# Kernel optimization log

Measured on AMD Instinct MI355X. Metric: run time of the kernel, lower is better.

## Reference

```python
import jax, jax.numpy as jnp
import numpy as np

NUM_HEADS = 16
D_MODEL = 1024
D_K = 64
D_V = 64
NEG_INF = -1e9


def setup_inputs() -> dict:
    key = jax.random.key(0)
    ks = jax.random.split(key, 7)
    B, S = 2, 2048
    Q = jax.random.normal(ks[0], (B, S, D_MODEL), dtype=jnp.float32)
    K = jax.random.normal(ks[1], (B, S, D_MODEL), dtype=jnp.float32)
    V = jax.random.normal(ks[2], (B, S, D_MODEL), dtype=jnp.float32)
    s = 1.0 / np.sqrt(D_MODEL)
    W_q = jax.random.normal(ks[3], (D_MODEL, D_K * NUM_HEADS), dtype=jnp.float32) * s
    W_k = jax.random.normal(ks[4], (D_MODEL, D_K), dtype=jnp.float32) * s
    W_v = jax.random.normal(ks[5], (D_MODEL, D_V), dtype=jnp.float32) * s
    W_o = jax.random.normal(ks[6], (D_V * NUM_HEADS, D_MODEL), dtype=jnp.float32) * (1.0 / np.sqrt(D_V * NUM_HEADS))
    return {"Q": Q, "K": K, "V": V, "W_q": W_q, "W_k": W_k, "W_v": W_v, "W_o": W_o}


def reference(Q, K, V, W_q, W_k, W_v, W_o):
    B, Sq, _ = Q.shape
    Sk = K.shape[1]
    # projections: Q -> per-head, K/V -> single shared head (MQA)
    q = (Q @ W_q).reshape(B, Sq, NUM_HEADS, D_K).transpose(0, 2, 1, 3)  # [B,H,Sq,Dk]
    k = K @ W_k  # [B,Sk,Dk]
    v = V @ W_v  # [B,Sk,Dv]
    scores = jnp.einsum('bhqd,bkd->bhqk', q, k) / jnp.sqrt(jnp.float32(D_K))
    causal = jnp.tril(jnp.ones((Sq, Sk), dtype=bool))  # [Sq,Sk]
    scores = jnp.where(causal[None, None], scores, NEG_INF)
    attn = jax.nn.softmax(scores, axis=-1)  # [B,H,Sq,Sk]
    out = jnp.einsum('bhqk,bkd->bhqd', attn, v)  # [B,H,Sq,Dv]
    out = out.transpose(0, 2, 1, 3).reshape(B, Sq, NUM_HEADS * D_V)
    return out @ W_o
```

## Files before the change

### kernel.cpp

```cpp
#include <hip/hip_runtime.h>
#include <hip/hip_bf16.h>
#include <cstdint>

typedef __bf16 bf16_t;
typedef __bf16 bf16x8 __attribute__((ext_vector_type(8)));
typedef __bf16 bf16x4 __attribute__((ext_vector_type(4)));
typedef float  floatx4 __attribute__((ext_vector_type(4)));

__device__ __forceinline__ bf16_t f2bf(float x) { return (bf16_t)x; }

__device__ __forceinline__ void gll16(const void* g, void* l) {
  __builtin_amdgcn_global_load_lds((const __attribute__((address_space(1))) void*)g,
                                   (__attribute__((address_space(3))) void*)l, 16, 0, 0);
}

#define S_LEN 2048
#define NHEAD 16
#define NTILE 32

__global__ __launch_bounds__(256) void transpose_w2(const float* __restrict__ W0,
                                                    const float* __restrict__ W1,
                                                    bf16_t* __restrict__ O0,
                                                    bf16_t* __restrict__ O1,
                                                    int K, int N) {
  const float* W = blockIdx.z ? W1 : W0;
  bf16_t* Wt = blockIdx.z ? O1 : O0;
  __shared__ float tile[32][33];
  int n0 = blockIdx.x * 32, k0 = blockIdx.y * 32;
  int tx = threadIdx.x & 31, ty = threadIdx.x >> 5;
#pragma unroll
  for (int r = 0; r < 4; ++r)
    tile[ty + 8 * r][tx] = W[(size_t)(k0 + ty + 8 * r) * N + n0 + tx];
  __syncthreads();
#pragma unroll
  for (int r = 0; r < 4; ++r)
    Wt[(size_t)(n0 + ty + 8 * r) * K + k0 + tx] = f2bf(tile[tx][ty + 8 * r]);
}

template <int OUTMODE, bool A_FP32>
__global__ __launch_bounds__(256, 2) void gemm_async(const void* __restrict__ Ain,
                                                     const bf16_t* __restrict__ Bt,
                                                     void* __restrict__ Cout,
                                                     int M, int N, int K) {
  constexpr int BK = 64;
  __shared__ __align__(16) bf16_t As[64 * BK];
  __shared__ __align__(16) bf16_t Bs[128 * BK];
  const int tid = threadIdx.x;
  const int wave = tid >> 6, lane = tid & 63;
  const int quad = lane >> 4, lm = lane & 15;
  const int wr = wave >> 1, wc = wave & 1;
  const int m0 = blockIdx.x * 64, n0 = blockIdx.y * 128;

  floatx4 acc[2][4];
#pragma unroll
  for (int i = 0; i < 2; ++i)
#pragma unroll
    for (int j = 0; j < 4; ++j) acc[i][j] = (floatx4){0.f, 0.f, 0.f, 0.f};

  for (int k0 = 0; k0 < K; k0 += BK) {
    if constexpr (A_FP32) {
#pragma unroll
      for (int rd = 0; rd < 2; ++rd) {
        int idx = rd * 256 + tid, row = idx >> 3, ch = (idx & 7) ^ (row & 7);
        const float* src = (const float*)Ain + (size_t)(m0 + row) * K + k0 + ch * 8;
        float4 f0 = *(const float4*)src;
        float4 f1 = *(const float4*)(src + 4);
        bf16x8 o;
        o[0] = f2bf(f0.x); o[1] = f2bf(f0.y); o[2] = f2bf(f0.z); o[3] = f2bf(f0.w);
        o[4] = f2bf(f1.x); o[5] = f2bf(f1.y); o[6] = f2bf(f1.z); o[7] = f2bf(f1.w);
        *(bf16x8*)&As[idx * 8] = o;
      }
    } else {
#pragma unroll
      for (int rd = 0; rd < 2; ++rd) {
        int idx = rd * 256 + tid, row = idx >> 3, ch = (idx & 7) ^ (row & 7);
        gll16((const bf16_t*)Ain + (size_t)(m0 + row) * K + k0 + ch * 8,
              As + (rd * 256 + wave * 64) * 8);
      }
    }
#pragma unroll
    for (int rd = 0; rd < 4; ++rd) {
      int idx = rd * 256 + tid, row = idx >> 3, ch = (idx & 7) ^ (row & 7);
      gll16(Bt + (size_t)(n0 + row) * K + k0 + ch * 8,
            Bs + (rd * 256 + wave * 64) * 8);
    }
    __syncthreads();
    const int sw = lm & 7;
    bf16x8 af[2][2], bfr[4][2];
#pragma unroll
    for (int i = 0; i < 2; ++i) {
      const bf16_t* base = &As[(wr * 32 + i * 16 + lm) * BK];
      af[i][0] = *(const bf16x8*)(base + ((quad ^ sw) * 8));
      af[i][1] = *(const bf16x8*)(base + (((4 + quad) ^ sw) * 8));
    }
#pragma unroll
    for (int j = 0; j < 4; ++j) {
      const bf16_t* base = &Bs[(wc * 64 + j * 16 + lm) * BK];
      bfr[j][0] = *(const bf16x8*)(base + ((quad ^ sw) * 8));
      bfr[j][1] = *(const bf16x8*)(base + (((4 + quad) ^ sw) * 8));
    }
#pragma unroll
    for (int ks = 0; ks < 2; ++ks)
#pragma unroll
      for (int i = 0; i < 2; ++i)
#pragma unroll
        for (int j = 0; j < 4; ++j)
          acc[i][j] = __builtin_amdgcn_mfma_f32_16x16x32_bf16(af[i][ks], bfr[j][ks],
                                                              acc[i][j], 0, 0, 0);
    __syncthreads();
  }
#pragma unroll
  for (int i = 0; i < 2; ++i) {
#pragma unroll
    for (int j = 0; j < 4; ++j) {
      int row0 = m0 + wr * 32 + i * 16 + quad * 4;
      int col = n0 + wc * 64 + j * 16 + lm;
#pragma unroll
      for (int r = 0; r < 4; ++r) {
        if constexpr (OUTMODE == 3)
          ((bf16_t*)Cout)[(size_t)(row0 + r) * N + col] = f2bf(acc[i][j][r] * 0.125f);
        else
          ((float*)Cout)[(size_t)(row0 + r) * N + col] = acc[i][j][r];
      }
    }
  }
}

__global__ __launch_bounds__(256) void gemm_kv(const float* __restrict__ Kin,
                                               const float* __restrict__ Vin,
                                               const bf16_t* __restrict__ Wkt,
                                               const bf16_t* __restrict__ Wvt,
                                               bf16_t* __restrict__ kp,
                                               bf16_t* __restrict__ vpt,
                                               int M, int K) {
  constexpr int BK = 32, LDK = 40, N = 64;
  const int isV = blockIdx.z;
  const float* A32 = isV ? Vin : Kin;
  const bf16_t* Bt = isV ? Wvt : Wkt;
  __shared__ __align__(16) bf16_t As[64 * LDK];
  __shared__ __align__(16) bf16_t Bs[64 * LDK];
  const int tid = threadIdx.x;
  const int wave = tid >> 6, lane = tid & 63;
  const int quad = lane >> 4, lm = lane & 15;
  const int wr = wave >> 1, wc = wave & 1;
  const int m0 = blockIdx.x * 64;

  floatx4 acc[2][2];
#pragma unroll
  for (int i = 0; i < 2; ++i)
#pragma unroll
    for (int j = 0; j < 2; ++j) acc[i][j] = (floatx4){0.f, 0.f, 0.f, 0.f};

  for (int k0 = 0; k0 < K; k0 += BK) {
    {
      int row = tid >> 2, c8 = tid & 3;
      const float* src = A32 + (size_t)(m0 + row) * K + k0 + c8 * 8;
      float4 f0 = *(const float4*)src;
      float4 f1 = *(const float4*)(src + 4);
      bf16x8 o;
      o[0] = f2bf(f0.x); o[1] = f2bf(f0.y); o[2] = f2bf(f0.z); o[3] = f2bf(f0.w);
      o[4] = f2bf(f1.x); o[5] = f2bf(f1.y); o[6] = f2bf(f1.z); o[7] = f2bf(f1.w);
      *(bf16x8*)&As[row * LDK + c8 * 8] = o;
    }
    {
      int row = tid >> 2, c8 = tid & 3;
      *(bf16x8*)&Bs[row * LDK + c8 * 8] =
          *(const bf16x8*)(Bt + (size_t)row * K + k0 + c8 * 8);
    }
    __syncthreads();
    bf16x8 af[2], bfr[2];
#pragma unroll
    for (int i = 0; i < 2; ++i)
      af[i] = *(const bf16x8*)&As[(wr * 32 + i * 16 + lm) * LDK + quad * 8];
#pragma unroll
    for (int j = 0; j < 2; ++j)
      bfr[j] = *(const bf16x8*)&Bs[(wc * 32 + j * 16 + lm) * LDK + quad * 8];
#pragma unroll
    for (int i = 0; i < 2; ++i)
#pragma unroll
      for (int j = 0; j < 2; ++j)
        acc[i][j] = __builtin_amdgcn_mfma_f32_16x16x32_bf16(af[i], bfr[j],
                                                            acc[i][j], 0, 0, 0);
    __syncthreads();
  }
#pragma unroll
  for (int i = 0; i < 2; ++i) {
#pragma unroll
    for (int j = 0; j < 2; ++j) {
      int row0 = m0 + wr * 32 + i * 16 + quad * 4;
      int col = wc * 32 + j * 16 + lm;
      if (isV) {
        bf16x4 o;
#pragma unroll
        for (int r = 0; r < 4; ++r) o[r] = f2bf(acc[i][j][r]);
        *(bf16x4*)&vpt[(size_t)col * M + row0] = o;
      } else {
#pragma unroll
        for (int r = 0; r < 4; ++r)
          kp[(size_t)(row0 + r) * N + col] = f2bf(acc[i][j][r]);
      }
    }
  }
}

__global__ __launch_bounds__(128, 2) void flash_mqa(const bf16_t* __restrict__ q,
                                                    const bf16_t* __restrict__ kk,
                                                    const bf16_t* __restrict__ vt,
                                                    bf16_t* __restrict__ O,
                                                    int BStot) {
  const int qt = NTILE - 1 - blockIdx.x;
  const int hb = blockIdx.y, b = blockIdx.z;
  const int tid = threadIdx.x;
  const int wave = tid >> 6, lane = tid & 63;
  const int quad = lane >> 4, lm = lane & 15;
  const int h = hb * 2 + wave;

  __shared__ __align__(16) bf16_t k_lds[2][64 * 64];
  __shared__ __align__(16) bf16_t v_lds[2][64 * 64];
  __shared__ __align__(16) bf16_t p_lds[2][64 * 64];

  const size_t bS = (size_t)b * S_LEN;
  const int qb = qt * 64;
  const int sw = lm & 7;

  bf16x8 qf[4][2];
#pragma unroll
  for (int m = 0; m < 4; ++m) {
    const bf16_t* qp = q + (bS + qb + m * 16 + lm) * 1024 + h * 64;
    qf[m][0] = *(const bf16x8*)(qp + quad * 8);
    qf[m][1] = *(const bf16x8*)(qp + 32 + quad * 8);
  }
  bf16x8 onesf;
#pragma unroll
  for (int j = 0; j < 8; ++j) onesf[j] = f2bf(1.0f);

  floatx4 acc[4][4];
  floatx4 ps[4];
#pragma unroll
  for (int m = 0; m < 4; ++m) {
    ps[m] = (floatx4){0.f, 0.f, 0.f, 0.f};
#pragma unroll
    for (int t = 0; t < 4; ++t) acc[m][t] = (floatx4){0.f, 0.f, 0.f, 0.f};
  }

  const int stid = tid;
  bf16x8 kst[4], vst[4];
  auto load_kv = [&](int kt) {
    const int k0 = kt * 64;
#pragma unroll
    for (int it = 0; it < 4; ++it) {
      int idx = it * 128 + stid, r = idx >> 3, c8 = idx & 7;
      kst[it] = *(const bf16x8*)(kk + (bS + k0 + r) * 64 + c8 * 8);
      vst[it] = *(const bf16x8*)(vt + (size_t)r * BStot + bS + k0 + c8 * 8);
    }
  };
  auto write_kv = [&](int buf) {
#pragma unroll
    for (int it = 0; it < 4; ++it) {
      int idx = it * 128 + stid, r = idx >> 3, c8 = idx & 7;
      int addr = r * 64 + ((c8 ^ (r & 7)) * 8);
      *(bf16x8*)&k_lds[buf][addr] = kst[it];
      *(bf16x8*)&v_lds[buf][addr] = vst[it];
    }
  };

  load_kv(0);
  write_kv(0);
  __syncthreads();

  for (int kt = 0; kt <= qt; ++kt) {
    const int cur = kt & 1;
    if (kt < qt) load_kv(kt + 1);

    const bool diag = (kt == qt);
#pragma unroll
    for (int t = 0; t < 4; ++t) {
      const bf16_t* kb = &k_lds[cur][(t * 16 + lm) * 64];
      bf16x8 a0 = *(const bf16x8*)(kb + ((quad ^ sw) * 8));
      bf16x8 a1 = *(const bf16x8*)(kb + (((4 + quad) ^ sw) * 8));
      floatx4 s[4];
#pragma unroll
      for (int m = 0; m < 4; ++m) {
        floatx4 cc = (floatx4){0.f, 0.f, 0.f, 0.f};
        cc = __builtin_amdgcn_mfma_f32_16x16x32_bf16(a0, qf[m][0], cc, 0, 0, 0);
        cc = __builtin_amdgcn_mfma_f32_16x16x32_bf16(a1, qf[m][1], cc, 0, 0, 0);
        s[m] = cc;
      }
      if (diag) {
#pragma unroll
        for (int m = 0; m < 4; ++m) {
          int qq = m * 16 + lm;
#pragma unroll
          for (int r = 0; r < 4; ++r) {
            int kj = t * 16 + quad * 4 + r;
            s[m][r] = (kj <= qq) ? __expf(s[m][r]) : 0.f;
          }
        }
      } else {
#pragma unroll
        for (int m = 0; m < 4; ++m)
#pragma unroll
          for (int r = 0; r < 4; ++r) s[m][r] = __expf(s[m][r]);
      }
#pragma unroll
      for (int m = 0; m < 4; ++m) {
        bf16x4 pk;
#pragma unroll
        for (int r = 0; r < 4; ++r) pk[r] = f2bf(s[m][r]);
        *(bf16x4*)&p_lds[wave][(m * 16 + lm) * 64 +
                               (((2 * t + (quad >> 1)) ^ sw) * 8) + (quad & 1) * 4] = pk;
      }
    }
    bf16x8 p0[4], p1[4];
#pragma unroll
    for (int m = 0; m < 4; ++m) {
      const bf16_t* pb = &p_lds[wave][(m * 16 + lm) * 64];
      p0[m] = *(const bf16x8*)(pb + ((quad ^ sw) * 8));
      p1[m] = *(const bf16x8*)(pb + (((4 + quad) ^ sw) * 8));
      ps[m] = __builtin_amdgcn_mfma_f32_16x16x32_bf16(p0[m], onesf, ps[m], 0, 0, 0);
      ps[m] = __builtin_amdgcn_mfma_f32_16x16x32_bf16(p1[m], onesf, ps[m], 0, 0, 0);
    }
#pragma unroll
    for (int t = 0; t < 4; ++t) {
      const bf16_t* vb = &v_lds[cur][(t * 16 + lm) * 64];
      bf16x8 v0 = *(const bf16x8*)(vb + ((quad ^ sw) * 8));
      bf16x8 v1 = *(const bf16x8*)(vb + (((4 + quad) ^ sw) * 8));
#pragma unroll
      for (int m = 0; m < 4; ++m) {
        acc[m][t] = __builtin_amdgcn_mfma_f32_16x16x32_bf16(p0[m], v0, acc[m][t], 0, 0, 0);
        acc[m][t] = __builtin_amdgcn_mfma_f32_16x16x32_bf16(p1[m], v1, acc[m][t], 0, 0, 0);
      }
    }
    if (kt < qt) write_kv(1 - cur);
    __syncthreads();
  }

#pragma unroll
  for (int m = 0; m < 4; ++m) {
    float rl[4];
#pragma unroll
    for (int r = 0; r < 4; ++r) rl[r] = 1.0f / ps[m][r];
    const int q0 = qb + m * 16 + quad * 4;
#pragma unroll
    for (int t = 0; t < 4; ++t)
#pragma unroll
      for (int r = 0; r < 4; ++r)
        O[(bS + q0 + r) * 1024 + h * 64 + t * 16 + lm] = f2bf(acc[m][t][r] * rl[r]);
  }
}

extern "C" void kernel_launch(void* const* d_in, const int* in_sizes, int n_in,
                              void* d_out, int out_size, void* d_ws, size_t ws_size,
                              hipStream_t stream) {
  const float* Q  = (const float*)d_in[0];
  const float* K  = (const float*)d_in[1];
  const float* V  = (const float*)d_in[2];
  const float* Wq = (const float*)d_in[3];
  const float* Wk = (const float*)d_in[4];
  const float* Wv = (const float*)d_in[5];
  const float* Wo = (const float*)d_in[6];

  const int BS = in_sizes[0] / 1024;
  const int B  = BS / S_LEN;

  bf16_t* ws  = (bf16_t*)d_ws;
  bf16_t* qp  = ws;
  bf16_t* Ob  = qp  + (size_t)BS * 1024;
  bf16_t* Wqt = Ob  + (size_t)BS * 1024;
  bf16_t* Wot = Wqt + (size_t)1024 * 1024;
  bf16_t* Wkt = Wot + (size_t)1024 * 1024;
  bf16_t* Wvt = Wkt + (size_t)64 * 1024;
  bf16_t* kp  = Wvt + (size_t)64 * 1024;
  bf16_t* vpt = kp  + (size_t)BS * 64;

  transpose_w2<<<dim3(32, 32, 2), 256, 0, stream>>>(Wq, Wo, Wqt, Wot, 1024, 1024);
  transpose_w2<<<dim3(2, 32, 2),  256, 0, stream>>>(Wk, Wv, Wkt, Wvt, 1024, 64);

  gemm_kv<<<dim3(BS / 64, 1, 2), 256, 0, stream>>>(K, V, Wkt, Wvt, kp, vpt, BS, 1024);

  gemm_async<3, true><<<dim3(BS / 64, 8), 256, 0, stream>>>(Q, Wqt, qp, BS, 1024, 1024);

  flash_mqa<<<dim3(NTILE, NHEAD / 2, B), 128, 0, stream>>>(qp, kp, vpt, Ob, BS);

  gemm_async<0, false><<<dim3(BS / 64, 8), 256, 0, stream>>>(Ob, Wot, (float*)d_out, BS, 1024, 1024);
}
```

Baseline: 236.6 us.

## Merge transpose and projection launches, retile flash attention to 32-row query tiles

Combines the two weight-transpose launches into one kernel and the Q and K/V projection GEMMs into one launch that dispatches on block index. This removes launch gaps and lets the small K/V projection overlap with the Q projection. The attention kernel now uses 32-query tiles with four heads per 256-thread block, so all four waves share each K/V tile load and the grid has finer causal work granularity. The diagonal mask is adjusted with an offset because a 32-row tile sits inside a 64-key tile. Each block now does half the per-wave MFMA work per K tile, so per-block overhead rises relative to compute.

Result: faster. 197.9 us (-16.3%).

```diff
diff --git a/kernel.cpp b/kernel.cpp
--- a/kernel.cpp
+++ b/kernel.cpp
@@ -16,17 +16,28 @@
 
 #define S_LEN 2048
 #define NHEAD 16
-#define NTILE 32
-
-__global__ __launch_bounds__(256) void transpose_w2(const float* __restrict__ W0,
-                                                    const float* __restrict__ W1,
-                                                    bf16_t* __restrict__ O0,
-                                                    bf16_t* __restrict__ O1,
-                                                    int K, int N) {
-  const float* W = blockIdx.z ? W1 : W0;
-  bf16_t* Wt = blockIdx.z ? O1 : O0;
+
+__global__ __launch_bounds__(256) void transpose_all(const float* __restrict__ Wq,
+                                                     const float* __restrict__ Wo,
+                                                     const float* __restrict__ Wk,
+                                                     const float* __restrict__ Wv,
+                                                     bf16_t* __restrict__ Wqt,
+                                                     bf16_t* __restrict__ Wot,
+                                                     bf16_t* __restrict__ Wkt,
+                                                     bf16_t* __restrict__ Wvt) {
+  const int bid = blockIdx.x;
+  const float* W; bf16_t* Wt; int n0, k0, N;
+  if (bid < 2048) {
+    int z = bid >> 10, rem = bid & 1023;
+    W = z ? Wo : Wq; Wt = z ? Wot : Wqt;
+    n0 = (rem & 31) * 32; k0 = (rem >> 5) * 32; N = 1024;
+  } else {
+    int b2 = bid - 2048, z = b2 >> 6, rem = b2 & 63;
+    W = z ? Wv : Wk; Wt = z ? Wvt : Wkt;
+    n0 = (rem & 1) * 32; k0 = (rem >> 1) * 32; N = 64;
+  }
+  const int K = 1024;
   __shared__ float tile[32][33];
-  int n0 = blockIdx.x * 32, k0 = blockIdx.y * 32;
   int tx = threadIdx.x & 31, ty = threadIdx.x >> 5;
 #pragma unroll
   for (int r = 0; r < 4; ++r)
@@ -38,18 +49,17 @@
 }
 
 template <int OUTMODE, bool A_FP32>
-__global__ __launch_bounds__(256, 2) void gemm_async(const void* __restrict__ Ain,
-                                                     const bf16_t* __restrict__ Bt,
-                                                     void* __restrict__ Cout,
-                                                     int M, int N, int K) {
+__device__ __forceinline__ void gemm_body(const void* __restrict__ Ain,
+                                          const bf16_t* __restrict__ Bt,
+                                          void* __restrict__ Cout,
+                                          int M, int N, int K,
+                                          int m0, int n0,
+                                          bf16_t* As, bf16_t* Bs) {
   constexpr int BK = 64;
-  __shared__ __align__(16) bf16_t As[64 * BK];
-  __shared__ __align__(16) bf16_t Bs[128 * BK];
   const int tid = threadIdx.x;
   const int wave = tid >> 6, lane = tid & 63;
   const int quad = lane >> 4, lm = lane & 15;
   const int wr = wave >> 1, wc = wave & 1;
-  const int m0 = blockIdx.x * 64, n0 = blockIdx.y * 128;
 
   floatx4 acc[2][4];
 #pragma unroll
@@ -126,24 +136,17 @@
   }
 }
 
-__global__ __launch_bounds__(256) void gemm_kv(const float* __restrict__ Kin,
-                                               const float* __restrict__ Vin,
-                                               const bf16_t* __restrict__ Wkt,
-                                               const bf16_t* __restrict__ Wvt,
-                                               bf16_t* __restrict__ kp,
-                                               bf16_t* __restrict__ vpt,
-                                               int M, int K) {
+__device__ __forceinline__ void kv_body(const float* __restrict__ A32,
+                                        const bf16_t* __restrict__ Bt,
+                                        bf16_t* __restrict__ kp,
+                                        bf16_t* __restrict__ vpt,
+                                        int M, int K, int m0, int isV,
+                                        bf16_t* As, bf16_t* Bs) {
   constexpr int BK = 32, LDK = 40, N = 64;
-  const int isV = blockIdx.z;
-  const float* A32 = isV ? Vin : Kin;
-  const bf16_t* Bt = isV ? Wvt : Wkt;
-  __shared__ __align__(16) bf16_t As[64 * LDK];
-  __shared__ __align__(16) bf16_t Bs[64 * LDK];
   const int tid = threadIdx.x;
   const int wave = tid >> 6, lane = tid & 63;
   const int quad = lane >> 4, lm = lane & 15;
   const int wr = wave >> 1, wc = wave & 1;
-  const int m0 = blockIdx.x * 64;
 
   floatx4 acc[2][2];
 #pragma unroll
@@ -203,29 +206,66 @@
   }
 }
 
-__global__ __launch_bounds__(128, 2) void flash_mqa(const bf16_t* __restrict__ q,
+__global__ __launch_bounds__(256, 2) void proj_all(const float* __restrict__ Q,
+                                                   const float* __restrict__ K,
+                                                   const float* __restrict__ V,
+                                                   const bf16_t* __restrict__ Wqt,
+                                                   const bf16_t* __restrict__ Wkt,
+                                                   const bf16_t* __restrict__ Wvt,
+                                                   bf16_t* __restrict__ qp,
+                                                   bf16_t* __restrict__ kp,
+                                                   bf16_t* __restrict__ vpt,
+                                                   int BS) {
+  __shared__ __align__(16) bf16_t As[64 * 64];
+  __shared__ __align__(16) bf16_t Bs[128 * 64];
+  const int bid = blockIdx.x;
+  const int nQ = (BS / 64) * 8;
+  if (bid < nQ) {
+    int m0 = (bid & (BS / 64 - 1)) * 64, n0 = (bid / (BS / 64)) * 128;
+    gemm_body<3, true>(Q, Wqt, qp, BS, 1024, 1024, m0, n0, As, Bs);
+  } else {
+    int b2 = bid - nQ;
+    int isV = (b2 >= BS / 64);
+    int m0 = (b2 & (BS / 64 - 1)) * 64;
+    kv_body(isV ? V : K, isV ? Wvt : Wkt, kp, vpt, BS, 1024, m0, isV, As, Bs);
+  }
+}
+
+__global__ __launch_bounds__(256, 2) void gemm_oproj(const bf16_t* __restrict__ A,
+                                                     const bf16_t* __restrict__ Bt,
+                                                     float* __restrict__ Cout,
+                                                     int M, int N, int K) {
+  __shared__ __align__(16) bf16_t As[64 * 64];
+  __shared__ __align__(16) bf16_t Bs[128 * 64];
+  gemm_body<0, false>(A, Bt, Cout, M, N, K,
+                      blockIdx.x * 64, blockIdx.y * 128, As, Bs);
+}
+
+__global__ __launch_bounds__(256, 2) void flash_mqa(const bf16_t* __restrict__ q,
                                                     const bf16_t* __restrict__ kk,
                                                     const bf16_t* __restrict__ vt,
                                                     bf16_t* __restrict__ O,
                                                     int BStot) {
-  const int qt = NTILE - 1 - blockIdx.x;
-  const int hb = blockIdx.y, b = blockIdx.z;
+  const int qt = 63 - blockIdx.x;
+  const int hg = blockIdx.y, b = blockIdx.z;
   const int tid = threadIdx.x;
   const int wave = tid >> 6, lane = tid & 63;
   const int quad = lane >> 4, lm = lane & 15;
-  const int h = hb * 2 + wave;
+  const int h = hg * 4 + wave;
 
   __shared__ __align__(16) bf16_t k_lds[2][64 * 64];
   __shared__ __align__(16) bf16_t v_lds[2][64 * 64];
-  __shared__ __align__(16) bf16_t p_lds[2][64 * 64];
+  __shared__ __align__(16) bf16_t p_lds[4][32 * 64];
 
   const size_t bS = (size_t)b * S_LEN;
-  const int qb = qt * 64;
+  const int qb = qt * 32;
+  const int ktmax = qt >> 1;
+  const int qoff = qb - ktmax * 64;
   const int sw = lm & 7;
 
-  bf16x8 qf[4][2];
-#pragma unroll
-  for (int m = 0; m < 4; ++m) {
+  bf16x8 qf[2][2];
+#pragma unroll
+  for (int m = 0; m < 2; ++m) {
     const bf16_t* qp = q + (bS + qb + m * 16 + lm) * 1024 + h * 64;
     qf[m][0] = *(const bf16x8*)(qp + quad * 8);
     qf[m][1] = *(const bf16x8*)(qp + 32 + quad * 8);
@@ -234,30 +274,29 @@
 #pragma unroll
   for (int j = 0; j < 8; ++j) onesf[j] = f2bf(1.0f);
 
-  floatx4 acc[4][4];
-  floatx4 ps[4];
-#pragma unroll
-  for (int m = 0; m < 4; ++m) {
+  floatx4 acc[2][4];
+  floatx4 ps[2];
+#pragma unroll
+  for (int m = 0; m < 2; ++m) {
     ps[m] = (floatx4){0.f, 0.f, 0.f, 0.f};
 #pragma unroll
     for (int t = 0; t < 4; ++t) acc[m][t] = (floatx4){0.f, 0.f, 0.f, 0.f};
   }
 
-  const int stid = tid;
-  bf16x8 kst[4], vst[4];
+  bf16x8 kst[2], vst[2];
   auto load_kv = [&](int kt) {
     const int k0 = kt * 64;
 #pragma unroll
-    for (int it = 0; it < 4; ++it) {
-      int idx = it * 128 + stid, r = idx >> 3, c8 = idx & 7;
+    for (int it = 0; it < 2; ++it) {
+      int idx = it * 256 + tid, r = idx >> 3, c8 = idx & 7;
       kst[it] = *(const bf16x8*)(kk + (bS + k0 + r) * 64 + c8 * 8);
       vst[it] = *(const bf16x8*)(vt + (size_t)r * BStot + bS + k0 + c8 * 8);
     }
   };
   auto write_kv = [&](int buf) {
 #pragma unroll
-    for (int it = 0; it < 4; ++it) {
-      int idx = it * 128 + stid, r = idx >> 3, c8 = idx & 7;
+    for (int it = 0; it < 2; ++it) {
+      int idx = it * 256 + tid, r = idx >> 3, c8 = idx & 7;
       int addr = r * 64 + ((c8 ^ (r & 7)) * 8);
       *(bf16x8*)&k_lds[buf][addr] = kst[it];
       *(bf16x8*)&v_lds[buf][addr] = vst[it];
@@ -268,19 +307,19 @@
   write_kv(0);
   __syncthreads();
 
-  for (int kt = 0; kt <= qt; ++kt) {
+  for (int kt = 0; kt <= ktmax; ++kt) {
     const int cur = kt & 1;
-    if (kt < qt) load_kv(kt + 1);
-
-    const bool diag = (kt == qt);
+    if (kt < ktmax) load_kv(kt + 1);
+    const bool diag = (kt == ktmax);
+
 #pragma unroll
     for (int t = 0; t < 4; ++t) {
       const bf16_t* kb = &k_lds[cur][(t * 16 + lm) * 64];
       bf16x8 a0 = *(const bf16x8*)(kb + ((quad ^ sw) * 8));
       bf16x8 a1 = *(const bf16x8*)(kb + (((4 + quad) ^ sw) * 8));
-      floatx4 s[4];
-#pragma unroll
-      for (int m = 0; m < 4; ++m) {
+      floatx4 s[2];
+#pragma unroll
+      for (int m = 0; m < 2; ++m) {
         floatx4 cc = (floatx4){0.f, 0.f, 0.f, 0.f};
         cc = __builtin_amdgcn_mfma_f32_16x16x32_bf16(a0, qf[m][0], cc, 0, 0, 0);
         cc = __builtin_amdgcn_mfma_f32_16x16x32_bf16(a1, qf[m][1], cc, 0, 0, 0);
@@ -288,8 +327,8 @@
       }
       if (diag) {
 #pragma unroll
-        for (int m = 0; m < 4; ++m) {
-          int qq = m * 16 + lm;
+        for (int m = 0; m < 2; ++m) {
+          int qq = qoff + m * 16 + lm;
 #pragma unroll
           for (int r = 0; r < 4; ++r) {
             int kj = t * 16 + quad * 4 + r;
@@ -298,12 +337,12 @@
         }
       } else {
 #pragma unroll
-        for (int m = 0; m < 4; ++m)
+        for (int m = 0; m < 2; ++m)
 #pragma unroll
           for (int r = 0; r < 4; ++r) s[m][r] = __expf(s[m][r]);
       }
 #pragma unroll
-      for (int m = 0; m < 4; ++m) {
+      for (int m = 0; m < 2; ++m) {
         bf16x4 pk;
 #pragma unroll
         for (int r = 0; r < 4; ++r) pk[r] = f2bf(s[m][r]);
@@ -311,9 +350,9 @@
                                (((2 * t + (quad >> 1)) ^ sw) * 8) + (quad & 1) * 4] = pk;
       }
     }
-    bf16x8 p0[4], p1[4];
-#pragma unroll
-    for (int m = 0; m < 4; ++m) {
+    bf16x8 p0[2], p1[2];
+#pragma unroll
+    for (int m = 0; m < 2; ++m) {
       const bf16_t* pb = &p_lds[wave][(m * 16 + lm) * 64];
       p0[m] = *(const bf16x8*)(pb + ((quad ^ sw) * 8));
       p1[m] = *(const bf16x8*)(pb + (((4 + quad) ^ sw) * 8));
@@ -326,17 +365,17 @@
       bf16x8 v0 = *(const bf16x8*)(vb + ((quad ^ sw) * 8));
       bf16x8 v1 = *(const bf16x8*)(vb + (((4 + quad) ^ sw) * 8));
 #pragma unroll
-      for (int m = 0; m < 4; ++m) {
+      for (int m = 0; m < 2; ++m) {
         acc[m][t] = __builtin_amdgcn_mfma_f32_16x16x32_bf16(p0[m], v0, acc[m][t], 0, 0, 0);
         acc[m][t] = __builtin_amdgcn_mfma_f32_16x16x32_bf16(p1[m], v1, acc[m][t], 0, 0, 0);
       }
     }
-    if (kt < qt) write_kv(1 - cur);
+    if (kt < ktmax) write_kv(1 - cur);
     __syncthreads();
   }
 
 #pragma unroll
-  for (int m = 0; m < 4; ++m) {
+  for (int m = 0; m < 2; ++m) {
     float rl[4];
 #pragma unroll
     for (int r = 0; r < 4; ++r) rl[r] = 1.0f / ps[m][r];
@@ -373,14 +412,12 @@
   bf16_t* kp  = Wvt + (size_t)64 * 1024;
   bf16_t* vpt = kp  + (size_t)BS * 64;
 
-  transpose_w2<<<dim3(32, 32, 2), 256, 0, stream>>>(Wq, Wo, Wqt, Wot, 1024, 1024);
-  transpose_w2<<<dim3(2, 32, 2),  256, 0, stream>>>(Wk, Wv, Wkt, Wvt, 1024, 64);
-
-  gemm_kv<<<dim3(BS / 64, 1, 2), 256, 0, stream>>>(K, V, Wkt, Wvt, kp, vpt, BS, 1024);
-
-  gemm_async<3, true><<<dim3(BS / 64, 8), 256, 0, stream>>>(Q, Wqt, qp, BS, 1024, 1024);
-
-  flash_mqa<<<dim3(NTILE, NHEAD / 2, B), 128, 0, stream>>>(qp, kp, vpt, Ob, BS);
-
-  gemm_async<0, false><<<dim3(BS / 64, 8), 256, 0, stream>>>(Ob, Wot, (float*)d_out, BS, 1024, 1024);
-}
+  transpose_all<<<2176, 256, 0, stream>>>(Wq, Wo, Wk, Wv, Wqt, Wot, Wkt, Wvt);
+
+  proj_all<<<(BS / 64) * 8 + (BS / 64) * 2, 256, 0, stream>>>(
+      Q, K, V, Wqt, Wkt, Wvt, qp, kp, vpt, BS);
+
+  flash_mqa<<<dim3(S_LEN / 32, NHEAD / 4, B), 256, 0, stream>>>(qp, kp, vpt, Ob, BS);
+
+  gemm_oproj<<<dim3(BS / 64, 8), 256, 0, stream>>>(Ob, Wot, (float*)d_out, BS, 1024, 1024);
+}
```
